# Performance work log

Measured on AMD Instinct MI355X. Metric: run time of the kernel, lower is better.

Reference implementation:

```python
import jax, jax.numpy as jnp
import numpy as np

D_MODEL = 1024
NUM_HEADS = 16
D_K = D_MODEL // NUM_HEADS
S, B = 2048, 2


def setup_inputs() -> dict:
    key = jax.random.key(0)
    ks = jax.random.split(key, 11)
    lim = 1.0 / np.sqrt(D_MODEL)
    def lin(kw, kb):
        W = jax.random.uniform(kw, (D_MODEL, D_MODEL), jnp.float32, -lim, lim)
        b = jax.random.uniform(kb, (D_MODEL,), jnp.float32, -lim, lim)
        return W, b
    Wq, bq = lin(ks[0], ks[1])
    Wk, bk = lin(ks[2], ks[3])
    Wv, bv = lin(ks[4], ks[5])
    Wo, bo = lin(ks[6], ks[7])
    q = jax.random.normal(ks[8], (S, B, D_MODEL), jnp.float32)
    k = jax.random.normal(ks[9], (S, B, D_MODEL), jnp.float32)
    v = jax.random.normal(ks[10], (S, B, D_MODEL), jnp.float32)
    return {"q": q, "k": k, "v": v,
            "Wq": Wq, "bq": bq, "Wk": Wk, "bk": bk,
            "Wv": Wv, "bv": bv, "Wo": Wo, "bo": bo}


def reference(q, k, v, Wq, bq, Wk, bk, Wv, bv, Wo, bo):
    s, b, _ = q.shape
    scale = np.sqrt(D_K).astype(np.float32)
    # torch Linear: x @ W.T + b
    def proj(x, W, bias):
        y = jnp.einsum('sbd,ed->sbe', x, W) + bias
        # [S,B,D] -> [B,H,S,d_k]
        return y.reshape(s, b, NUM_HEADS, D_K).transpose(1, 2, 0, 3)
    Q = proj(q, Wq, bq)
    K = proj(k, Wk, bk)
    V = proj(v, Wv, bv)
    scores = jnp.einsum('bhsd,bhtd->bhst', Q, K) / scale  # [B,H,S,S]
    attn = jax.nn.softmax(scores, axis=-1)
    ctx = jnp.einsum('bhst,bhtd->bhsd', attn, V)  # [B,H,S,d_k]
    ctx = ctx.transpose(2, 0, 1, 3).reshape(s, b, NUM_HEADS * D_K)
    return jnp.einsum('sbd,ed->sbe', ctx, Wo) + bo
```

## Files before the change

kernel.cpp:

```cpp
#include <hip/hip_runtime.h>
#include <stdint.h>

typedef __attribute__((ext_vector_type(8))) short short8;
typedef __attribute__((ext_vector_type(4))) float f32x4;
typedef __attribute__((ext_vector_type(16))) float f32x16;

#define MFMA16(a, b, c) __builtin_amdgcn_mfma_f32_16x16x32_bf16((a), (b), (c), 0, 0, 0)
#define MFMA32(a, b, c) __builtin_amdgcn_mfma_f32_32x32x16_bf16((a), (b), (c), 0, 0, 0)

__device__ inline unsigned short f2bf(float x) {
  unsigned u = __float_as_uint(x);
  u = (u + 0x7FFFu + ((u >> 16) & 1u)) >> 16;
  return (unsigned short)u;
}

__device__ inline void gload16(const unsigned short* g, unsigned short* l) {
  __builtin_amdgcn_global_load_lds(
      (const __attribute__((address_space(1))) unsigned int*)g,
      (__attribute__((address_space(3))) unsigned int*)l, 16, 0, 0);
}

__device__ inline short8 lds8(const unsigned short* base, int byteoff) {
  return *reinterpret_cast<const short8*>(reinterpret_cast<const char*>(base) + byteoff);
}

__device__ inline unsigned cvtpk(float lo, float hi) {
  unsigned r;
  asm("v_cvt_pk_bf16_f32 %0, %1, %2" : "=v"(r) : "v"(lo), "v"(hi));
  return r;
}
__device__ inline void plswap(unsigned& a, unsigned& b) {
  asm volatile("v_permlane32_swap_b32 %0, %1" : "+v"(a), "+v"(b));
}
__device__ inline float swapadd(float v) {
  float a = v, b;
  asm volatile("v_mov_b32 %1, %0\n\tv_permlane32_swap_b32 %0, %1" : "+v"(a), "=&v"(b));
  return a + b;
}

__device__ inline short8 mk8(unsigned a, unsigned b, unsigned c, unsigned d) {
  union { unsigned u[4]; short8 v; } x;
  x.u[0] = a; x.u[1] = b; x.u[2] = c; x.u[3] = d;
  return x.v;
}

__device__ inline int swz(int row, int chunk) {
  return row * 128 + (((chunk) ^ (row & 7)) << 4);
}

__device__ inline void exppack(const f32x16& sv, float& lsum, short8& paLo, short8& paHi) {
  float p[16];
#pragma unroll
  for (int i = 0; i < 16; ++i) p[i] = __builtin_amdgcn_exp2f(sv[i]);
  float q8[8];
#pragma unroll
  for (int i = 0; i < 8; ++i) q8[i] = p[2 * i] + p[2 * i + 1];
#pragma unroll
  for (int s2 = 4; s2 > 0; s2 >>= 1)
#pragma unroll
    for (int i = 0; i < s2; ++i) q8[i] += q8[i + s2];
  lsum += q8[0];
  unsigned w0 = cvtpk(p[0], p[1]), w1 = cvtpk(p[2], p[3]);
  unsigned w2 = cvtpk(p[4], p[5]), w3 = cvtpk(p[6], p[7]);
  plswap(w0, w2); plswap(w1, w3);
  unsigned w4 = cvtpk(p[8], p[9]), w5 = cvtpk(p[10], p[11]);
  unsigned w6 = cvtpk(p[12], p[13]), w7 = cvtpk(p[14], p[15]);
  plswap(w4, w6); plswap(w5, w7);
  paLo = mk8(w0, w1, w2, w3);
  paHi = mk8(w4, w5, w6, w7);
}

__global__ __launch_bounds__(256) void cvt_bf16x(const float* __restrict__ a0,
                                                 const float* __restrict__ a1,
                                                 const float* __restrict__ a2,
                                                 const float* __restrict__ a3,
                                                 unsigned short* __restrict__ d, int per) {
  int y = blockIdx.y;
  const float* s = (y == 0) ? a0 : (y == 1) ? a1 : (y == 2) ? a2 : a3;
  int i = (blockIdx.x * 256 + threadIdx.x) * 8;
  if (i >= per) return;
  float4 v0 = *reinterpret_cast<const float4*>(s + i);
  float4 v1 = *reinterpret_cast<const float4*>(s + i + 4);
  short8 o;
  o[0] = (short)f2bf(v0.x); o[1] = (short)f2bf(v0.y);
  o[2] = (short)f2bf(v0.z); o[3] = (short)f2bf(v0.w);
  o[4] = (short)f2bf(v1.x); o[5] = (short)f2bf(v1.y);
  o[6] = (short)f2bf(v1.z); o[7] = (short)f2bf(v1.w);
  *reinterpret_cast<short8*>(d + (size_t)y * per + i) = o;
}

template <int MODE>
__global__ __launch_bounds__(256) void gemm_bt(
    const unsigned short* __restrict__ Abase, const unsigned short* __restrict__ Wbase,
    const float* __restrict__ bias0, const float* __restrict__ bias1,
    const float* __restrict__ bias2, unsigned short* __restrict__ ObaseBf,
    float* __restrict__ ObaseF, int M, int N, int K) {
  constexpr int CHUNK = (MODE == 0) ? 192 : 64;

  const int orig = blockIdx.x;
  const int wg = (orig & 7) * CHUNK + (orig >> 3);
  int z, bx, by;
  if (MODE == 0) {
    z = wg >> 9;
    int r = wg & 511;
    by = r & 15;
    bx = r >> 4;
  } else {
    z = 0; by = wg & 15; bx = wg >> 4;
  }

  const unsigned short* A = Abase + (size_t)z * M * K;
  const unsigned short* W = Wbase + (size_t)z * N * K;
  const float* bias = (z == 0) ? bias0 : (z == 1 ? bias1 : bias2);

  __shared__ unsigned short As[2 * 128 * 64];
  __shared__ unsigned short Bs[2 * 64 * 64];

  const int t = threadIdx.x;
  const int lane = t & 63, w = t >> 6;
  const int wm = w >> 1, wn = w & 1;
  const int m0 = bx * 128, n0 = by * 64;
  const int lrow = lane & 15, lg = lane >> 4;

  f32x4 acc[4][2] = {};

  int arow[4], acol[4], brow[2], bcol[2];
#pragma unroll
  for (int p = 0; p < 4; ++p) {
    int c = (p * 4 + w) * 64 + lane;
    arow[p] = c >> 3; acol[p] = ((c & 7) ^ (arow[p] & 7)) * 8;
  }
#pragma unroll
  for (int p = 0; p < 2; ++p) {
    int c = (p * 4 + w) * 64 + lane;
    brow[p] = c >> 3; bcol[p] = ((c & 7) ^ (brow[p] & 7)) * 8;
  }

#define STAGE_G(kt, buf)                                                              \
  {                                                                                   \
    _Pragma("unroll") for (int p = 0; p < 4; ++p)                                     \
        gload16(&A[(size_t)(m0 + arow[p]) * K + (kt) + acol[p]],                      \
                &As[(buf)*8192 + ((p * 4 + w) * 64) * 8]);                            \
    _Pragma("unroll") for (int p = 0; p < 2; ++p)                                     \
        gload16(&W[(size_t)(n0 + brow[p]) * K + (kt) + bcol[p]],                      \
                &Bs[(buf)*4096 + ((p * 4 + w) * 64) * 8]);                            \
  }

#define COMPUTE(buf)                                                                  \
  {                                                                                   \
    _Pragma("unroll") for (int kc = 0; kc < 2; ++kc) {                                \
      short8 af[4], bfr[2];                                                           \
      _Pragma("unroll") for (int i = 0; i < 4; ++i)                                   \
          af[i] = lds8(As, (buf)*16384 + swz(wm * 64 + i * 16 + lrow, kc * 4 + lg));  \
      _Pragma("unroll") for (int i = 0; i < 2; ++i)                                   \
          bfr[i] = lds8(Bs, (buf)*8192 + swz(wn * 32 + i * 16 + lrow, kc * 4 + lg));  \
      _Pragma("unroll") for (int mi = 0; mi < 4; ++mi)                                \
          _Pragma("unroll") for (int ni = 0; ni < 2; ++ni)                            \
              acc[mi][ni] = MFMA16(af[mi], bfr[ni], acc[mi][ni]);                     \
    }                                                                                 \
  }

  STAGE_G(0, 0);
  asm volatile("s_waitcnt vmcnt(0)" ::: "memory");
  __builtin_amdgcn_s_barrier();
  __builtin_amdgcn_sched_barrier(0);

  int cur = 0;
  for (int kt = 0; kt < K - 64; kt += 64) {
    STAGE_G(kt + 64, cur ^ 1);
    COMPUTE(cur);
    asm volatile("s_waitcnt vmcnt(0)" ::: "memory");
    __builtin_amdgcn_s_barrier();
    __builtin_amdgcn_sched_barrier(0);
    cur ^= 1;
  }
  COMPUTE(cur);
#undef STAGE_G
#undef COMPUTE

  const int r0 = lg * 4;
  if (MODE == 0) {
    const float scale = (z == 0) ? 0.18033688011112042f : 1.0f;
    if (z < 2) {
      unsigned short* O = ObaseBf + (size_t)z * (size_t)M * N;
#pragma unroll
      for (int mi = 0; mi < 4; ++mi)
#pragma unroll
        for (int ni = 0; ni < 2; ++ni) {
          int e = n0 + wn * 32 + ni * 16 + lrow;
          float be = bias[e];
          int h = e >> 6, d = e & 63;
#pragma unroll
          for (int r = 0; r < 4; ++r) {
            int m = m0 + wm * 64 + mi * 16 + r0 + r;
            int s = m >> 1, bb = m & 1;
            O[(((size_t)(bb * 16 + h) * 2048 + s) << 6) + d] = f2bf((acc[mi][ni][r] + be) * scale);
          }
        }
    } else {
      unsigned short* O = ObaseBf + (size_t)2 * (size_t)M * N;
#pragma unroll
      for (int mi = 0; mi < 4; ++mi)
#pragma unroll
        for (int ni = 0; ni < 2; ++ni) {
          int e = n0 + wn * 32 + ni * 16 + lrow;
          float be = bias[e];
          int h = e >> 6, d = e & 63;
#pragma unroll
          for (int r = 0; r < 4; ++r) {
            int m = m0 + wm * 64 + mi * 16 + r0 + r;
            int s = m >> 1, bb = m & 1;
            O[(((size_t)(bb * 16 + h) * 64 + d) << 11) + s] = f2bf(acc[mi][ni][r] + be);
          }
        }
    }
  } else {
    float* O = ObaseF;
#pragma unroll
    for (int mi = 0; mi < 4; ++mi)
#pragma unroll
      for (int ni = 0; ni < 2; ++ni) {
        int e = n0 + wn * 32 + ni * 16 + lrow;
        float be = bias[e];
#pragma unroll
        for (int r = 0; r < 4; ++r) {
          int m = m0 + wm * 64 + mi * 16 + r0 + r;
          O[(size_t)m * N + e] = acc[mi][ni][r] + be;
        }
      }
  }
}

__global__ __launch_bounds__(256, 2) void attn(const unsigned short* __restrict__ Q,
                                               const unsigned short* __restrict__ K,
                                               const unsigned short* __restrict__ Vt,
                                               unsigned short* __restrict__ ctx) {
  __shared__ unsigned short Ks[4 * 4096];
  __shared__ unsigned short Vs[4 * 4096];

  const int orig = blockIdx.x;
  const int wg = ((orig & 7) << 6) + (orig >> 3);
  const int bh = wg >> 4;
  const int qb = wg & 15;

  const int t = threadIdx.x, lane = t & 63, wv = t >> 6;
  const int q0 = qb * 128 + wv * 32;
  const int q = lane & 31, hi = lane >> 5;
  const int fq = (q ^ (q >> 3)) & 7;

  const unsigned short* Qb = Q + ((size_t)bh * 2048 + q0) * 64;
  const unsigned short* Kb = K + (size_t)bh * 2048 * 64;
  const unsigned short* Vb = Vt + (size_t)bh * 64 * 2048;

  short8 qf[4];
#pragma unroll
  for (int m = 0; m < 4; ++m)
    qf[m] = *reinterpret_cast<const short8*>(&Qb[q * 64 + m * 16 + hi * 8]);

  int koff[2][4], voff[2][2][2];
#pragma unroll
  for (int st = 0; st < 2; ++st) {
    int f = fq ^ (st ? 4 : 0);
#pragma unroll
    for (int m = 0; m < 4; ++m)
      koff[st][m] = (st * 32 + q) * 128 + (((m * 2 + hi) ^ f) << 4);
  }
#pragma unroll
  for (int dh = 0; dh < 2; ++dh) {
    int f = fq ^ (dh ? 4 : 0);
#pragma unroll
    for (int st = 0; st < 2; ++st)
#pragma unroll
      for (int kc = 0; kc < 2; ++kc)
        voff[dh][st][kc] = (dh * 32 + q) * 128 + (((st * 4 + kc * 2 + hi) ^ f) << 4);
  }

  int c0 = wv * 64 + lane, c1 = (4 + wv) * 64 + lane;
  int sr0 = c0 >> 3, sr1 = c1 >> 3;
  int sc0c = ((c0 & 7) ^ ((sr0 ^ (sr0 >> 3)) & 7)) * 8;
  int sc1c = ((c1 & 7) ^ ((sr1 ^ (sr1 >> 3)) & 7)) * 8;
  const unsigned short* ks0 = Kb + (size_t)sr0 * 64 + sc0c;
  const unsigned short* ks1 = Kb + (size_t)sr1 * 64 + sc1c;
  const unsigned short* vp0 = Vb + (size_t)sr0 * 2048 + sc0c;
  const unsigned short* vp1 = Vb + (size_t)sr1 * 2048 + sc1c;

#define STAGE(tt)                                                      \
  {                                                                    \
    char* kb = (char*)Ks + ((tt) & 3) * 8192;                          \
    char* vb2 = (char*)Vs + ((tt) & 3) * 8192;                         \
    gload16(ks0, (unsigned short*)(kb + wv * 1024));                   \
    gload16(ks1, (unsigned short*)(kb + (4 + wv) * 1024));             \
    gload16(vp0, (unsigned short*)(vb2 + wv * 1024));                  \
    gload16(vp1, (unsigned short*)(vb2 + (4 + wv) * 1024));            \
    ks0 += 4096; ks1 += 4096; vp0 += 64; vp1 += 64;                    \
  }

  f32x16 oa0 = {}, oa1 = {};
  float lsum = 0.f;
  const f32x16 zero16 = {};
  f32x16 sA0 = {}, sA1 = {}, sB0, sB1;

  STAGE(0); STAGE(1); STAGE(2);
  asm volatile("s_waitcnt vmcnt(8)" ::: "memory");
  __builtin_amdgcn_s_barrier();
  __builtin_amdgcn_sched_barrier(0);
#pragma unroll
  for (int m = 0; m < 4; ++m) {
    sA0 = MFMA32(lds8(Ks, koff[0][m]), qf[m], sA0);
    sA1 = MFMA32(lds8(Ks, koff[1][m]), qf[m], sA1);
  }

#define PHASE(tcur, sC0, sC1, sN0, sN1)                                         \
  {                                                                             \
    asm volatile("s_waitcnt vmcnt(4)" ::: "memory");                            \
    __builtin_amdgcn_sched_barrier(0);                                          \
    __builtin_amdgcn_s_barrier();                                               \
    __builtin_amdgcn_sched_barrier(0);                                          \
    STAGE((tcur) + 3);                                                          \
    sN0 = zero16; sN1 = zero16;                                                 \
    __builtin_amdgcn_s_setprio(1);                                              \
    {                                                                           \
      const int so = (((tcur) + 1) & 3) * 8192;                                 \
      _Pragma("unroll") for (int m = 0; m < 4; ++m) {                           \
        sN0 = MFMA32(lds8(Ks, so + koff[0][m]), qf[m], sN0);                    \
        sN1 = MFMA32(lds8(Ks, so + koff[1][m]), qf[m], sN1);                    \
      }                                                                         \
    }                                                                           \
    short8 paL0, paH0, paL1, paH1;                                              \
    exppack(sC0, lsum, paL0, paH0);                                             \
    exppack(sC1, lsum, paL1, paH1);                                             \
    {                                                                           \
      const int vo = ((tcur) & 3) * 8192;                                       \
      oa0 = MFMA32(paL0, lds8(Vs, vo + voff[0][0][0]), oa0);                    \
      oa1 = MFMA32(paL0, lds8(Vs, vo + voff[1][0][0]), oa1);                    \
      oa0 = MFMA32(paH0, lds8(Vs, vo + voff[0][0][1]), oa0);                    \
      oa1 = MFMA32(paH0, lds8(Vs, vo + voff[1][0][1]), oa1);                    \
      oa0 = MFMA32(paL1, lds8(Vs, vo + voff[0][1][0]), oa0);                    \
      oa1 = MFMA32(paL1, lds8(Vs, vo + voff[1][1][0]), oa1);                    \
      oa0 = MFMA32(paH1, lds8(Vs, vo + voff[0][1][1]), oa0);                    \
      oa1 = MFMA32(paH1, lds8(Vs, vo + voff[1][1][1]), oa1);                    \
    }                                                                           \
    __builtin_amdgcn_s_setprio(0);                                              \
  }

  for (int it = 0; it < 15; ++it) {
    int tc = 2 * it;
    PHASE(tc, sA0, sA1, sB0, sB1);
    PHASE(tc + 1, sB0, sB1, sA0, sA1);
  }
  PHASE(30, sA0, sA1, sB0, sB1);

  {
    short8 paL0, paH0, paL1, paH1;
    exppack(sB0, lsum, paL0, paH0);
    exppack(sB1, lsum, paL1, paH1);
    const int vo = 3 * 8192;
    oa0 = MFMA32(paL0, lds8(Vs, vo + voff[0][0][0]), oa0);
    oa1 = MFMA32(paL0, lds8(Vs, vo + voff[1][0][0]), oa1);
    oa0 = MFMA32(paH0, lds8(Vs, vo + voff[0][0][1]), oa0);
    oa1 = MFMA32(paH0, lds8(Vs, vo + voff[1][0][1]), oa1);
    oa0 = MFMA32(paL1, lds8(Vs, vo + voff[0][1][0]), oa0);
    oa1 = MFMA32(paL1, lds8(Vs, vo + voff[1][1][0]), oa1);
    oa0 = MFMA32(paH1, lds8(Vs, vo + voff[0][1][1]), oa0);
    oa1 = MFMA32(paH1, lds8(Vs, vo + voff[1][1][1]), oa1);
  }
#undef PHASE
#undef STAGE

  lsum = swapadd(lsum);
  float linv = 1.0f / lsum;
  const int b = bh >> 4, h = bh & 15;
#pragma unroll
  for (int r = 0; r < 16; ++r) {
    int qr = (r & 3) + 8 * (r >> 2) + 4 * hi;
    float li = __shfl(linv, qr);
    size_t base = ((size_t)(q0 + qr) * 2 + b) * 1024 + h * 64 + q;
    ctx[base] = f2bf(oa0[r] * li);
    ctx[base + 32] = f2bf(oa1[r] * li);
  }
}

extern "C" void kernel_launch(void* const* d_in, const int* in_sizes, int n_in, void* d_out,
                              int out_size, void* d_ws, size_t ws_size, hipStream_t stream) {
  const float* q  = (const float*)d_in[0];
  const float* k  = (const float*)d_in[1];
  const float* v  = (const float*)d_in[2];
  const float* Wq = (const float*)d_in[3];
  const float* bq = (const float*)d_in[4];
  const float* Wk = (const float*)d_in[5];
  const float* bk = (const float*)d_in[6];
  const float* Wv = (const float*)d_in[7];
  const float* bv = (const float*)d_in[8];
  const float* Wo = (const float*)d_in[9];
  const float* bo = (const float*)d_in[10];

  const size_t SZ_IN = 4194304;
  const size_t SZ_W  = 1048576;
  unsigned short* ws  = (unsigned short*)d_ws;
  unsigned short* xb  = ws;
  unsigned short* Wb  = xb + 3 * SZ_IN;
  unsigned short* QKV = Wb + 4 * SZ_W;
  unsigned short* ctx = QKV + 3 * SZ_IN;

  cvt_bf16x<<<dim3(SZ_IN / 2048, 3), 256, 0, stream>>>(q, k, v, v, xb, (int)SZ_IN);
  cvt_bf16x<<<dim3(SZ_W / 2048, 4), 256, 0, stream>>>(Wq, Wk, Wv, Wo, Wb, (int)SZ_W);

  gemm_bt<0><<<1536, 256, 0, stream>>>(xb, Wb, bq, bk, bv, QKV, nullptr, 4096, 1024, 1024);
  attn<<<512, 256, 0, stream>>>(QKV, QKV + SZ_IN, QKV + 2 * SZ_IN, ctx);
  gemm_bt<1><<<512, 256, 0, stream>>>(ctx, Wb + 3 * SZ_W, bo, bo, bo, nullptr,
                                      (float*)d_out, 4096, 1024, 1024);
}
```

Baseline: 124.2 us.

## Split attention over key halves with a separate combine kernel

Splits each attention work-group's key range into two halves (split-K/flash-decoding style), doubling the grid to 1024 blocks, and writes unnormalized fp32 partial outputs and row sums to workspace. A new combine kernel sums the two partials, normalizes and writes bf16 ctx. LDS pipelining drops from 4-stage to 2-stage double buffering with a full vmcnt(0) wait each tile, and launch bounds rise to 4 blocks per CU for more occupancy. This trades extra fp32 global traffic, an extra launch, and a less deeply pipelined loop for more parallelism. It relies on the exp not subtracting a running max, since partials are summed directly.

```diff
diff --git a/kernel.cpp b/kernel.cpp
--- a/kernel.cpp
+++ b/kernel.cpp
@@ -231,17 +231,19 @@
   }
 }
 
-__global__ __launch_bounds__(256, 2) void attn(const unsigned short* __restrict__ Q,
+__global__ __launch_bounds__(256, 4) void attn(const unsigned short* __restrict__ Q,
                                                const unsigned short* __restrict__ K,
                                                const unsigned short* __restrict__ Vt,
-                                               unsigned short* __restrict__ ctx) {
-  __shared__ unsigned short Ks[4 * 4096];
-  __shared__ unsigned short Vs[4 * 4096];
+                                               float* __restrict__ oaP,
+                                               float* __restrict__ lsumP) {
+  __shared__ unsigned short Ks[2 * 4096];
+  __shared__ unsigned short Vs[2 * 4096];
 
   const int orig = blockIdx.x;
-  const int wg = ((orig & 7) << 6) + (orig >> 3);
-  const int bh = wg >> 4;
-  const int qb = wg & 15;
+  const int wg = ((orig & 7) << 7) + (orig >> 3);
+  const int bh = wg >> 5;
+  const int qb = (wg >> 1) & 15;
+  const int kh = wg & 1;
 
   const int t = threadIdx.x, lane = t & 63, wv = t >> 6;
   const int q0 = qb * 128 + wv * 32;
@@ -249,8 +251,8 @@
   const int fq = (q ^ (q >> 3)) & 7;
 
   const unsigned short* Qb = Q + ((size_t)bh * 2048 + q0) * 64;
-  const unsigned short* Kb = K + (size_t)bh * 2048 * 64;
-  const unsigned short* Vb = Vt + (size_t)bh * 64 * 2048;
+  const unsigned short* Kb = K + ((size_t)bh * 2048 + kh * 1024) * 64;
+  const unsigned short* Vb = Vt + (size_t)bh * 64 * 2048 + kh * 1024;
 
   short8 qf[4];
 #pragma unroll
@@ -286,8 +288,8 @@
 
 #define STAGE(tt)                                                      \
   {                                                                    \
-    char* kb = (char*)Ks + ((tt) & 3) * 8192;                          \
-    char* vb2 = (char*)Vs + ((tt) & 3) * 8192;                         \
+    char* kb = (char*)Ks + ((tt) & 1) * 8192;                          \
+    char* vb2 = (char*)Vs + ((tt) & 1) * 8192;                         \
     gload16(ks0, (unsigned short*)(kb + wv * 1024));                   \
     gload16(ks1, (unsigned short*)(kb + (4 + wv) * 1024));             \
     gload16(vp0, (unsigned short*)(vb2 + wv * 1024));                  \
@@ -297,87 +299,77 @@
 
   f32x16 oa0 = {}, oa1 = {};
   float lsum = 0.f;
-  const f32x16 zero16 = {};
-  f32x16 sA0 = {}, sA1 = {}, sB0, sB1;
-
-  STAGE(0); STAGE(1); STAGE(2);
-  asm volatile("s_waitcnt vmcnt(8)" ::: "memory");
+
+  STAGE(0);
+  asm volatile("s_waitcnt vmcnt(0)" ::: "memory");
   __builtin_amdgcn_s_barrier();
   __builtin_amdgcn_sched_barrier(0);
-#pragma unroll
-  for (int m = 0; m < 4; ++m) {
-    sA0 = MFMA32(lds8(Ks, koff[0][m]), qf[m], sA0);
-    sA1 = MFMA32(lds8(Ks, koff[1][m]), qf[m], sA1);
-  }
-
-#define PHASE(tcur, sC0, sC1, sN0, sN1)                                         \
-  {                                                                             \
-    asm volatile("s_waitcnt vmcnt(4)" ::: "memory");                            \
-    __builtin_amdgcn_sched_barrier(0);                                          \
-    __builtin_amdgcn_s_barrier();                                               \
-    __builtin_amdgcn_sched_barrier(0);                                          \
-    STAGE((tcur) + 3);                                                          \
-    sN0 = zero16; sN1 = zero16;                                                 \
-    __builtin_amdgcn_s_setprio(1);                                              \
-    {                                                                           \
-      const int so = (((tcur) + 1) & 3) * 8192;                                 \
-      _Pragma("unroll") for (int m = 0; m < 4; ++m) {                           \
-        sN0 = MFMA32(lds8(Ks, so + koff[0][m]), qf[m], sN0);                    \
-        sN1 = MFMA32(lds8(Ks, so + koff[1][m]), qf[m], sN1);                    \
-      }                                                                         \
-    }                                                                           \
-    short8 paL0, paH0, paL1, paH1;                                              \
-    exppack(sC0, lsum, paL0, paH0);                                             \
-    exppack(sC1, lsum, paL1, paH1);                                             \
-    {                                                                           \
-      const int vo = ((tcur) & 3) * 8192;                                       \
-      oa0 = MFMA32(paL0, lds8(Vs, vo + voff[0][0][0]), oa0);                    \
-      oa1 = MFMA32(paL0, lds8(Vs, vo + voff[1][0][0]), oa1);                    \
-      oa0 = MFMA32(paH0, lds8(Vs, vo + voff[0][0][1]), oa0);                    \
-      oa1 = MFMA32(paH0, lds8(Vs, vo + voff[1][0][1]), oa1);                    \
-      oa0 = MFMA32(paL1, lds8(Vs, vo + voff[0][1][0]), oa0);                    \
-      oa1 = MFMA32(paL1, lds8(Vs, vo + voff[1][1][0]), oa1);                    \
-      oa0 = MFMA32(paH1, lds8(Vs, vo + voff[0][1][1]), oa0);                    \
-      oa1 = MFMA32(paH1, lds8(Vs, vo + voff[1][1][1]), oa1);                    \
-    }                                                                           \
-    __builtin_amdgcn_s_setprio(0);                                              \
-  }
-
-  for (int it = 0; it < 15; ++it) {
-    int tc = 2 * it;
-    PHASE(tc, sA0, sA1, sB0, sB1);
-    PHASE(tc + 1, sB0, sB1, sA0, sA1);
-  }
-  PHASE(30, sA0, sA1, sB0, sB1);
-
-  {
+
+  for (int tile = 0; tile < 16; ++tile) {
+    if (tile < 15) STAGE(tile + 1);
+    const int cur = (tile & 1) * 8192;
+    __builtin_amdgcn_s_setprio(1);
+
+    f32x16 s0 = {}, s1 = {};
+#pragma unroll
+    for (int m = 0; m < 4; ++m) {
+      s0 = MFMA32(lds8(Ks, cur + koff[0][m]), qf[m], s0);
+      s1 = MFMA32(lds8(Ks, cur + koff[1][m]), qf[m], s1);
+    }
+
     short8 paL0, paH0, paL1, paH1;
-    exppack(sB0, lsum, paL0, paH0);
-    exppack(sB1, lsum, paL1, paH1);
-    const int vo = 3 * 8192;
-    oa0 = MFMA32(paL0, lds8(Vs, vo + voff[0][0][0]), oa0);
-    oa1 = MFMA32(paL0, lds8(Vs, vo + voff[1][0][0]), oa1);
-    oa0 = MFMA32(paH0, lds8(Vs, vo + voff[0][0][1]), oa0);
-    oa1 = MFMA32(paH0, lds8(Vs, vo + voff[1][0][1]), oa1);
-    oa0 = MFMA32(paL1, lds8(Vs, vo + voff[0][1][0]), oa0);
-    oa1 = MFMA32(paL1, lds8(Vs, vo + voff[1][1][0]), oa1);
-    oa0 = MFMA32(paH1, lds8(Vs, vo + voff[0][1][1]), oa0);
-    oa1 = MFMA32(paH1, lds8(Vs, vo + voff[1][1][1]), oa1);
-  }
-#undef PHASE
+    exppack(s0, lsum, paL0, paH0);
+    exppack(s1, lsum, paL1, paH1);
+
+    oa0 = MFMA32(paL0, lds8(Vs, cur + voff[0][0][0]), oa0);
+    oa1 = MFMA32(paL0, lds8(Vs, cur + voff[1][0][0]), oa1);
+    oa0 = MFMA32(paH0, lds8(Vs, cur + voff[0][0][1]), oa0);
+    oa1 = MFMA32(paH0, lds8(Vs, cur + voff[1][0][1]), oa1);
+    oa0 = MFMA32(paL1, lds8(Vs, cur + voff[0][1][0]), oa0);
+    oa1 = MFMA32(paL1, lds8(Vs, cur + voff[1][1][0]), oa1);
+    oa0 = MFMA32(paH1, lds8(Vs, cur + voff[0][1][1]), oa0);
+    oa1 = MFMA32(paH1, lds8(Vs, cur + voff[1][1][1]), oa1);
+    __builtin_amdgcn_s_setprio(0);
+
+    if (tile < 15) {
+      asm volatile("s_waitcnt vmcnt(0)" ::: "memory");
+      __builtin_amdgcn_sched_barrier(0);
+      __builtin_amdgcn_s_barrier();
+      __builtin_amdgcn_sched_barrier(0);
+    }
+  }
 #undef STAGE
 
   lsum = swapadd(lsum);
-  float linv = 1.0f / lsum;
-  const int b = bh >> 4, h = bh & 15;
+  float* oaB = oaP + ((size_t)(kh * 32 + bh) * 2048 + q0) * 64;
 #pragma unroll
   for (int r = 0; r < 16; ++r) {
     int qr = (r & 3) + 8 * (r >> 2) + 4 * hi;
-    float li = __shfl(linv, qr);
-    size_t base = ((size_t)(q0 + qr) * 2 + b) * 1024 + h * 64 + q;
-    ctx[base] = f2bf(oa0[r] * li);
-    ctx[base + 32] = f2bf(oa1[r] * li);
-  }
+    size_t base = (size_t)qr * 64 + (lane & 31);
+    oaB[base] = oa0[r];
+    oaB[base + 32] = oa1[r];
+  }
+  if (lane < 32) lsumP[(size_t)(kh * 32 + bh) * 2048 + q0 + lane] = lsum;
+}
+
+__global__ __launch_bounds__(256) void combine(const float* __restrict__ oaP,
+                                               const float* __restrict__ lsumP,
+                                               unsigned short* __restrict__ ctx) {
+  int idx = blockIdx.x * 256 + threadIdx.x;
+  int e4 = idx << 2;
+  int bh = e4 >> 17;
+  int rem = e4 & 131071;
+  int qr = rem >> 6, d = rem & 63;
+  float4 lo = *reinterpret_cast<const float4*>(oaP + e4);
+  float4 hi = *reinterpret_cast<const float4*>(oaP + 4194304 + e4);
+  float inv = 1.0f / (lsumP[(size_t)bh * 2048 + qr] + lsumP[65536 + (size_t)bh * 2048 + qr]);
+  int b = bh >> 4, h = bh & 15;
+  ushort4 o;
+  o.x = f2bf((lo.x + hi.x) * inv);
+  o.y = f2bf((lo.y + hi.y) * inv);
+  o.z = f2bf((lo.z + hi.z) * inv);
+  o.w = f2bf((lo.w + hi.w) * inv);
+  *reinterpret_cast<ushort4*>(&ctx[((size_t)qr * 2 + b) * 1024 + h * 64 + d]) = o;
 }
 
 extern "C" void kernel_launch(void* const* d_in, const int* in_sizes, int n_in, void* d_out,
@@ -396,17 +388,20 @@
 
   const size_t SZ_IN = 4194304;
   const size_t SZ_W  = 1048576;
-  unsigned short* ws  = (unsigned short*)d_ws;
-  unsigned short* xb  = ws;
-  unsigned short* Wb  = xb + 3 * SZ_IN;
-  unsigned short* QKV = Wb + 4 * SZ_W;
-  unsigned short* ctx = QKV + 3 * SZ_IN;
+  char* wsb = (char*)d_ws;
+  unsigned short* xb  = (unsigned short*)wsb;
+  float* oaP          = (float*)wsb;
+  unsigned short* Wb  = (unsigned short*)(wsb + 33816576);
+  float* lsumP        = (float*)(wsb + 42205184);
+  unsigned short* QKV = (unsigned short*)(wsb + 42729472);
+  unsigned short* ctx = QKV;
 
   cvt_bf16x<<<dim3(SZ_IN / 2048, 3), 256, 0, stream>>>(q, k, v, v, xb, (int)SZ_IN);
   cvt_bf16x<<<dim3(SZ_W / 2048, 4), 256, 0, stream>>>(Wq, Wk, Wv, Wo, Wb, (int)SZ_W);
 
   gemm_bt<0><<<1536, 256, 0, stream>>>(xb, Wb, bq, bk, bv, QKV, nullptr, 4096, 1024, 1024);
-  attn<<<512, 256, 0, stream>>>(QKV, QKV + SZ_IN, QKV + 2 * SZ_IN, ctx);
+  attn<<<1024, 256, 0, stream>>>(QKV, QKV + SZ_IN, QKV + 2 * SZ_IN, oaP, lsumP);
+  combine<<<4096, 256, 0, stream>>>(oaP, lsumP, ctx);
   gemm_bt<1><<<512, 256, 0, stream>>>(ctx, Wb + 3 * SZ_W, bo, bo, bo, nullptr,
                                       (float*)d_out, 4096, 1024, 1024);
 }
```

New measurement: 133.6 us. 1.08x slower.

## Load GEMM weight fragments straight to registers and widen N tile to 128

Applied to the files above, without the earlier changes.

The projection GEMMs stop staging the weight operand in LDS. Each wave now loads its B fragments directly from global memory into registers, double-buffered across two register sets alongside the LDS double-buffered A tile. The N tile grows to 128 (and M shrinks to 64 for the output GEMM), so the QKV launch halves its block count. This removes LDS traffic and barriers for B and raises MFMA work per A fragment. In exchange, register pressure goes up and the direct global loads of B are uncoalesced.

```diff
diff --git a/kernel.cpp b/kernel.cpp
--- a/kernel.cpp
+++ b/kernel.cpp
@@ -95,87 +95,100 @@
     const float* __restrict__ bias0, const float* __restrict__ bias1,
     const float* __restrict__ bias2, unsigned short* __restrict__ ObaseBf,
     float* __restrict__ ObaseF, int M, int N, int K) {
-  constexpr int CHUNK = (MODE == 0) ? 192 : 64;
+  constexpr int BM = (MODE == 0) ? 128 : 64;
+  constexpr int WM = BM / 32;
+  constexpr int AP = BM / 32;
+  constexpr int CHUNK = (MODE == 0) ? 96 : 64;
 
   const int orig = blockIdx.x;
   const int wg = (orig & 7) * CHUNK + (orig >> 3);
   int z, bx, by;
   if (MODE == 0) {
-    z = wg >> 9;
-    int r = wg & 511;
-    by = r & 15;
-    bx = r >> 4;
+    z = wg >> 8;
+    int r = wg & 255;
+    by = r & 7;
+    bx = r >> 3;
   } else {
-    z = 0; by = wg & 15; bx = wg >> 4;
+    z = 0; by = wg & 7; bx = wg >> 3;
   }
 
   const unsigned short* A = Abase + (size_t)z * M * K;
   const unsigned short* W = Wbase + (size_t)z * N * K;
   const float* bias = (z == 0) ? bias0 : (z == 1 ? bias1 : bias2);
 
-  __shared__ unsigned short As[2 * 128 * 64];
-  __shared__ unsigned short Bs[2 * 64 * 64];
+  __shared__ unsigned short As[2 * BM * 64];
 
   const int t = threadIdx.x;
   const int lane = t & 63, w = t >> 6;
   const int wm = w >> 1, wn = w & 1;
-  const int m0 = bx * 128, n0 = by * 64;
+  const int m0 = bx * BM, n0 = by * 128;
   const int lrow = lane & 15, lg = lane >> 4;
 
-  f32x4 acc[4][2] = {};
-
-  int arow[4], acol[4], brow[2], bcol[2];
-#pragma unroll
-  for (int p = 0; p < 4; ++p) {
+  f32x4 acc[WM][4] = {};
+
+  int arow[AP], acol[AP];
+#pragma unroll
+  for (int p = 0; p < AP; ++p) {
     int c = (p * 4 + w) * 64 + lane;
     arow[p] = c >> 3; acol[p] = ((c & 7) ^ (arow[p] & 7)) * 8;
   }
-#pragma unroll
-  for (int p = 0; p < 2; ++p) {
-    int c = (p * 4 + w) * 64 + lane;
-    brow[p] = c >> 3; bcol[p] = ((c & 7) ^ (brow[p] & 7)) * 8;
-  }
-
-#define STAGE_G(kt, buf)                                                              \
+  const size_t bwoff = (size_t)(n0 + wn * 64 + lrow) * K + lg * 8;
+
+#define STAGE_A(kt, buf)                                                              \
   {                                                                                   \
-    _Pragma("unroll") for (int p = 0; p < 4; ++p)                                     \
+    _Pragma("unroll") for (int p = 0; p < AP; ++p)                                    \
         gload16(&A[(size_t)(m0 + arow[p]) * K + (kt) + acol[p]],                      \
-                &As[(buf)*8192 + ((p * 4 + w) * 64) * 8]);                            \
-    _Pragma("unroll") for (int p = 0; p < 2; ++p)                                     \
-        gload16(&W[(size_t)(n0 + brow[p]) * K + (kt) + bcol[p]],                      \
-                &Bs[(buf)*4096 + ((p * 4 + w) * 64) * 8]);                            \
-  }
-
-#define COMPUTE(buf)                                                                  \
+                &As[(buf)*BM * 64 + ((p * 4 + w) * 64) * 8]);                         \
+  }
+
+#define LOADB(kt, dst)                                                                \
+  {                                                                                   \
+    _Pragma("unroll") for (int ni = 0; ni < 4; ++ni)                                  \
+        _Pragma("unroll") for (int kc = 0; kc < 2; ++kc)                              \
+            dst[ni * 2 + kc] = *reinterpret_cast<const short8*>(                      \
+                &W[bwoff + (size_t)(ni * 16) * K + (kt) + kc * 32]);                  \
+  }
+
+#define COMPUTE(buf, b)                                                               \
   {                                                                                   \
     _Pragma("unroll") for (int kc = 0; kc < 2; ++kc) {                                \
-      short8 af[4], bfr[2];                                                           \
-      _Pragma("unroll") for (int i = 0; i < 4; ++i)                                   \
-          af[i] = lds8(As, (buf)*16384 + swz(wm * 64 + i * 16 + lrow, kc * 4 + lg));  \
-      _Pragma("unroll") for (int i = 0; i < 2; ++i)                                   \
-          bfr[i] = lds8(Bs, (buf)*8192 + swz(wn * 32 + i * 16 + lrow, kc * 4 + lg));  \
-      _Pragma("unroll") for (int mi = 0; mi < 4; ++mi)                                \
-          _Pragma("unroll") for (int ni = 0; ni < 2; ++ni)                            \
-              acc[mi][ni] = MFMA16(af[mi], bfr[ni], acc[mi][ni]);                     \
+      short8 af[WM];                                                                  \
+      _Pragma("unroll") for (int mi = 0; mi < WM; ++mi)                               \
+          af[mi] = lds8(As, (buf)*BM * 128 + swz(wm * (BM / 2) + mi * 16 + lrow,      \
+                                                 kc * 4 + lg));                       \
+      _Pragma("unroll") for (int mi = 0; mi < WM; ++mi)                               \
+          _Pragma("unroll") for (int ni = 0; ni < 4; ++ni)                            \
+              acc[mi][ni] = MFMA16(af[mi], b[ni * 2 + kc], acc[mi][ni]);              \
     }                                                                                 \
   }
 
-  STAGE_G(0, 0);
+  short8 bA[8], bB[8];
+
+  STAGE_A(0, 0);
+  LOADB(0, bA);
   asm volatile("s_waitcnt vmcnt(0)" ::: "memory");
   __builtin_amdgcn_s_barrier();
   __builtin_amdgcn_sched_barrier(0);
 
-  int cur = 0;
-  for (int kt = 0; kt < K - 64; kt += 64) {
-    STAGE_G(kt + 64, cur ^ 1);
-    COMPUTE(cur);
+  const int nit = K / 128;
+  for (int it = 0; it < nit; ++it) {
+    const int kt0 = it * 128;
+    STAGE_A(kt0 + 64, 1);
+    LOADB(kt0 + 64, bB);
+    COMPUTE(0, bA);
     asm volatile("s_waitcnt vmcnt(0)" ::: "memory");
     __builtin_amdgcn_s_barrier();
     __builtin_amdgcn_sched_barrier(0);
-    cur ^= 1;
-  }
-  COMPUTE(cur);
-#undef STAGE_G
+    const int ktn = (it + 1 < nit) ? kt0 + 128 : 0;
+    STAGE_A(ktn, 0);
+    LOADB(ktn, bA);
+    COMPUTE(1, bB);
+    asm volatile("s_waitcnt vmcnt(0)" ::: "memory");
+    __builtin_amdgcn_s_barrier();
+    __builtin_amdgcn_sched_barrier(0);
+  }
+#undef STAGE_A
+#undef LOADB
 #undef COMPUTE
 
   const int r0 = lg * 4;
@@ -184,15 +197,15 @@
     if (z < 2) {
       unsigned short* O = ObaseBf + (size_t)z * (size_t)M * N;
 #pragma unroll
-      for (int mi = 0; mi < 4; ++mi)
-#pragma unroll
-        for (int ni = 0; ni < 2; ++ni) {
-          int e = n0 + wn * 32 + ni * 16 + lrow;
+      for (int mi = 0; mi < WM; ++mi)
+#pragma unroll
+        for (int ni = 0; ni < 4; ++ni) {
+          int e = n0 + wn * 64 + ni * 16 + lrow;
           float be = bias[e];
           int h = e >> 6, d = e & 63;
 #pragma unroll
           for (int r = 0; r < 4; ++r) {
-            int m = m0 + wm * 64 + mi * 16 + r0 + r;
+            int m = m0 + wm * (BM / 2) + mi * 16 + r0 + r;
             int s = m >> 1, bb = m & 1;
             O[(((size_t)(bb * 16 + h) * 2048 + s) << 6) + d] = f2bf((acc[mi][ni][r] + be) * scale);
           }
@@ -200,15 +213,15 @@
     } else {
       unsigned short* O = ObaseBf + (size_t)2 * (size_t)M * N;
 #pragma unroll
-      for (int mi = 0; mi < 4; ++mi)
-#pragma unroll
-        for (int ni = 0; ni < 2; ++ni) {
-          int e = n0 + wn * 32 + ni * 16 + lrow;
+      for (int mi = 0; mi < WM; ++mi)
+#pragma unroll
+        for (int ni = 0; ni < 4; ++ni) {
+          int e = n0 + wn * 64 + ni * 16 + lrow;
           float be = bias[e];
           int h = e >> 6, d = e & 63;
 #pragma unroll
           for (int r = 0; r < 4; ++r) {
-            int m = m0 + wm * 64 + mi * 16 + r0 + r;
+            int m = m0 + wm * (BM / 2) + mi * 16 + r0 + r;
             int s = m >> 1, bb = m & 1;
             O[(((size_t)(bb * 16 + h) * 64 + d) << 11) + s] = f2bf(acc[mi][ni][r] + be);
           }
@@ -217,14 +230,14 @@
   } else {
     float* O = ObaseF;
 #pragma unroll
-    for (int mi = 0; mi < 4; ++mi)
-#pragma unroll
-      for (int ni = 0; ni < 2; ++ni) {
-        int e = n0 + wn * 32 + ni * 16 + lrow;
+    for (int mi = 0; mi < WM; ++mi)
+#pragma unroll
+      for (int ni = 0; ni < 4; ++ni) {
+        int e = n0 + wn * 64 + ni * 16 + lrow;
         float be = bias[e];
 #pragma unroll
         for (int r = 0; r < 4; ++r) {
-          int m = m0 + wm * 64 + mi * 16 + r0 + r;
+          int m = m0 + wm * (BM / 2) + mi * 16 + r0 + r;
           O[(size_t)m * N + e] = acc[mi][ni][r] + be;
         }
       }
@@ -405,7 +418,7 @@
   cvt_bf16x<<<dim3(SZ_IN / 2048, 3), 256, 0, stream>>>(q, k, v, v, xb, (int)SZ_IN);
   cvt_bf16x<<<dim3(SZ_W / 2048, 4), 256, 0, stream>>>(Wq, Wk, Wv, Wo, Wb, (int)SZ_W);
 
-  gemm_bt<0><<<1536, 256, 0, stream>>>(xb, Wb, bq, bk, bv, QKV, nullptr, 4096, 1024, 1024);
+  gemm_bt<0><<<768, 256, 0, stream>>>(xb, Wb, bq, bk, bv, QKV, nullptr, 4096, 1024, 1024);
   attn<<<512, 256, 0, stream>>>(QKV, QKV + SZ_IN, QKV + 2 * SZ_IN, ctx);
   gemm_bt<1><<<512, 256, 0, stream>>>(ctx, Wb + 3 * SZ_W, bo, bo, bo, nullptr,
                                       (float*)d_out, 4096, 1024, 1024);
```

New measurement: 187.9 us. +51.2%, slower.

## Fuse fp32-to-bf16 activation conversion into QKV projection GEMM A-tile staging

Applied to the files above, without the earlier changes.

Drops the separate kernel that converted q/k/v activations to bf16. The QKV GEMM now loads fp32 A tiles into registers, converts them to bf16, and writes them into the swizzled LDS buffer, while the weight tiles still use direct global-to-LDS loads. This removes a full write and re-read of the bf16 activation buffers and one launch. In exchange, the GEMM reads twice the bytes per A tile, uses extra registers, and adds an LDS write and wait step to the pipeline.

```diff
diff --git a/kernel.cpp b/kernel.cpp
--- a/kernel.cpp
+++ b/kernel.cpp
@@ -91,7 +91,8 @@
 
 template <int MODE>
 __global__ __launch_bounds__(256) void gemm_bt(
-    const unsigned short* __restrict__ Abase, const unsigned short* __restrict__ Wbase,
+    const float* __restrict__ Aq, const float* __restrict__ Ak, const float* __restrict__ Av,
+    const unsigned short* __restrict__ Abf, const unsigned short* __restrict__ Wbase,
     const float* __restrict__ bias0, const float* __restrict__ bias1,
     const float* __restrict__ bias2, unsigned short* __restrict__ ObaseBf,
     float* __restrict__ ObaseF, int M, int N, int K) {
@@ -109,7 +110,7 @@
     z = 0; by = wg & 15; bx = wg >> 4;
   }
 
-  const unsigned short* A = Abase + (size_t)z * M * K;
+  const float* A32 = (z == 0) ? Aq : (z == 1 ? Ak : Av);
   const unsigned short* W = Wbase + (size_t)z * N * K;
   const float* bias = (z == 0) ? bias0 : (z == 1 ? bias1 : bias2);
 
@@ -124,11 +125,11 @@
 
   f32x4 acc[4][2] = {};
 
-  int arow[4], acol[4], brow[2], bcol[2];
+  int arow[4], achk[4], brow[2], bcol[2];
 #pragma unroll
   for (int p = 0; p < 4; ++p) {
     int c = (p * 4 + w) * 64 + lane;
-    arow[p] = c >> 3; acol[p] = ((c & 7) ^ (arow[p] & 7)) * 8;
+    arow[p] = c >> 3; achk[p] = c & 7;
   }
 #pragma unroll
   for (int p = 0; p < 2; ++p) {
@@ -136,11 +137,36 @@
     brow[p] = c >> 3; bcol[p] = ((c & 7) ^ (brow[p] & 7)) * 8;
   }
 
-#define STAGE_G(kt, buf)                                                              \
+  float4 av0[4], av1[4];
+
+#define LOADA32(kt)                                                                   \
+  {                                                                                   \
+    _Pragma("unroll") for (int p = 0; p < 4; ++p) {                                   \
+      const float* src = &A32[(size_t)(m0 + arow[p]) * K + (kt) + achk[p] * 8];       \
+      av0[p] = *reinterpret_cast<const float4*>(src);                                 \
+      av1[p] = *reinterpret_cast<const float4*>(src + 4);                             \
+    }                                                                                 \
+  }
+
+#define WRITEA(buf)                                                                   \
   {                                                                                   \
     _Pragma("unroll") for (int p = 0; p < 4; ++p)                                     \
-        gload16(&A[(size_t)(m0 + arow[p]) * K + (kt) + acol[p]],                      \
-                &As[(buf)*8192 + ((p * 4 + w) * 64) * 8]);                            \
+        *reinterpret_cast<short8*>((char*)As + (buf)*16384 + swz(arow[p], achk[p])) = \
+            mk8(cvtpk(av0[p].x, av0[p].y), cvtpk(av0[p].z, av0[p].w),                 \
+                cvtpk(av1[p].x, av1[p].y), cvtpk(av1[p].z, av1[p].w));                \
+  }
+
+#define STAGE_ABF(kt, buf)                                                            \
+  {                                                                                   \
+    _Pragma("unroll") for (int p = 0; p < 4; ++p) {                                   \
+      int cc = achk[p] ^ (arow[p] & 7);                                               \
+      gload16(&Abf[(size_t)(m0 + arow[p]) * K + (kt) + cc * 8],                       \
+              &As[(buf)*8192 + ((p * 4 + w) * 64) * 8]);                              \
+    }                                                                                 \
+  }
+
+#define STAGE_W(kt, buf)                                                              \
+  {                                                                                   \
     _Pragma("unroll") for (int p = 0; p < 2; ++p)                                     \
         gload16(&W[(size_t)(n0 + brow[p]) * K + (kt) + bcol[p]],                      \
                 &Bs[(buf)*4096 + ((p * 4 + w) * 64) * 8]);                            \
@@ -160,22 +186,45 @@
     }                                                                                 \
   }
 
-  STAGE_G(0, 0);
-  asm volatile("s_waitcnt vmcnt(0)" ::: "memory");
+  if (MODE == 0) {
+    LOADA32(0);
+    STAGE_W(0, 0);
+    asm volatile("s_waitcnt vmcnt(0)" ::: "memory");
+    WRITEA(0);
+    asm volatile("s_waitcnt lgkmcnt(0)" ::: "memory");
+  } else {
+    STAGE_ABF(0, 0);
+    STAGE_W(0, 0);
+    asm volatile("s_waitcnt vmcnt(0)" ::: "memory");
+  }
   __builtin_amdgcn_s_barrier();
   __builtin_amdgcn_sched_barrier(0);
 
   int cur = 0;
   for (int kt = 0; kt < K - 64; kt += 64) {
-    STAGE_G(kt + 64, cur ^ 1);
-    COMPUTE(cur);
-    asm volatile("s_waitcnt vmcnt(0)" ::: "memory");
+    if (MODE == 0) {
+      LOADA32(kt + 64);
+      STAGE_W(kt + 64, cur ^ 1);
+      __builtin_amdgcn_sched_barrier(0);
+      COMPUTE(cur);
+      asm volatile("s_waitcnt vmcnt(0)" ::: "memory");
+      WRITEA(cur ^ 1);
+      asm volatile("s_waitcnt lgkmcnt(0)" ::: "memory");
+    } else {
+      STAGE_ABF(kt + 64, cur ^ 1);
+      STAGE_W(kt + 64, cur ^ 1);
+      COMPUTE(cur);
+      asm volatile("s_waitcnt vmcnt(0)" ::: "memory");
+    }
     __builtin_amdgcn_s_barrier();
     __builtin_amdgcn_sched_barrier(0);
     cur ^= 1;
   }
   COMPUTE(cur);
-#undef STAGE_G
+#undef LOADA32
+#undef WRITEA
+#undef STAGE_ABF
+#undef STAGE_W
 #undef COMPUTE
 
   const int r0 = lg * 4;
@@ -397,16 +446,15 @@
   const size_t SZ_IN = 4194304;
   const size_t SZ_W  = 1048576;
   unsigned short* ws  = (unsigned short*)d_ws;
-  unsigned short* xb  = ws;
-  unsigned short* Wb  = xb + 3 * SZ_IN;
+  unsigned short* Wb  = ws;
   unsigned short* QKV = Wb + 4 * SZ_W;
   unsigned short* ctx = QKV + 3 * SZ_IN;
 
-  cvt_bf16x<<<dim3(SZ_IN / 2048, 3), 256, 0, stream>>>(q, k, v, v, xb, (int)SZ_IN);
   cvt_bf16x<<<dim3(SZ_W / 2048, 4), 256, 0, stream>>>(Wq, Wk, Wv, Wo, Wb, (int)SZ_W);
 
-  gemm_bt<0><<<1536, 256, 0, stream>>>(xb, Wb, bq, bk, bv, QKV, nullptr, 4096, 1024, 1024);
+  gemm_bt<0><<<1536, 256, 0, stream>>>(q, k, v, nullptr, Wb, bq, bk, bv, QKV, nullptr,
+                                       4096, 1024, 1024);
   attn<<<512, 256, 0, stream>>>(QKV, QKV + SZ_IN, QKV + 2 * SZ_IN, ctx);
-  gemm_bt<1><<<512, 256, 0, stream>>>(ctx, Wb + 3 * SZ_W, bo, bo, bo, nullptr,
-                                      (float*)d_out, 4096, 1024, 1024);
-}
+  gemm_bt<1><<<512, 256, 0, stream>>>(nullptr, nullptr, nullptr, ctx, Wb + 3 * SZ_W,
+                                      bo, bo, bo, nullptr, (float*)d_out, 4096, 1024, 1024);
+}
```

After: 127.6 us. 1.03x slower.
